# Kernel optimization log

Measured on AMD Instinct MI355X. Metric: run time of the kernel, lower is better.

## Reference

```python
import jax, jax.numpy as jnp
import numpy as np

B, S, D = 2, 2048, 2048
H = 16
Q_LORA, KV_LORA = 1536, 512
D_NOPE, D_ROPE, D_V = 128, 64, 128
QK_D = D_NOPE + D_ROPE  # 192
EPS = 1e-6
ROPE_THETA = 10000.0


def rms_norm(x, w, eps=EPS):
    return x * jax.lax.rsqrt(jnp.mean(x * x, axis=-1, keepdims=True) + eps) * w


def apply_rope(x, cos, sin):
    # x: [b, s, h, d]; cos/sin: [s, d//2]; pairs are interleaved (x0,x1),(x2,x3),...
    xr, xi = x[..., 0::2], x[..., 1::2]
    c = cos[None, :, None, :]
    s = sin[None, :, None, :]
    yr = xr * c - xi * s
    yi = xr * s + xi * c
    return jnp.stack([yr, yi], axis=-1).reshape(x.shape)


def setup_inputs() -> dict:
    key = jax.random.key(0)
    ks = jax.random.split(key, 8)
    sd = 0.02
    pos = jnp.arange(S, dtype=jnp.float32)
    inv_freq = 1.0 / (ROPE_THETA ** (jnp.arange(0, D_ROPE, 2, dtype=jnp.float32) / D_ROPE))
    ang = pos[:, None] * inv_freq[None, :]  # [S, D_ROPE//2]
    mask = jnp.triu(jnp.full((S, S), float('-inf'), dtype=jnp.float32), k=1)
    return {
        'x': jax.random.normal(ks[0], (B, S, D), dtype=jnp.float32),
        'freqs_cos': jnp.cos(ang),
        'freqs_sin': jnp.sin(ang),
        'mask': mask,
        'wq_a': jax.random.normal(ks[1], (Q_LORA, D), dtype=jnp.float32) * sd,
        'q_norm_w': jnp.ones((Q_LORA,), dtype=jnp.float32),
        'wq_b': jax.random.normal(ks[2], (H * QK_D, Q_LORA), dtype=jnp.float32) * sd,
        'wkv_a': jax.random.normal(ks[3], (KV_LORA + D_ROPE, D), dtype=jnp.float32) * sd,
        'kv_norm_w': jnp.ones((KV_LORA,), dtype=jnp.float32),
        'wkv_b': jax.random.normal(ks[4], (H * (D_NOPE + D_V), KV_LORA), dtype=jnp.float32) * sd,
        'wo': jax.random.normal(ks[5], (D, H * D_V), dtype=jnp.float32) * sd,
    }


def reference(x, freqs_cos, freqs_sin, mask, wq_a, q_norm_w, wq_b, wkv_a, kv_norm_w, wkv_b, wo):
    b, s, _ = x.shape
    # query path: down-proj -> RMSNorm -> up-proj
    q = rms_norm(x @ wq_a.T, q_norm_w) @ wq_b.T          # [b, s, H*QK_D]
    q = q.reshape(b, s, H, QK_D)
    q_nope, q_pe = q[..., :D_NOPE], q[..., D_NOPE:]
    q_pe = apply_rope(q_pe, freqs_cos, freqs_sin)
    # kv path: joint down-proj, split latent / rope key
    kv_full = x @ wkv_a.T                                 # [b, s, KV_LORA + D_ROPE]
    kv, k_pe = kv_full[..., :KV_LORA], kv_full[..., KV_LORA:]
    k_pe = apply_rope(k_pe[:, :, None, :], freqs_cos, freqs_sin)  # [b, s, 1, D_ROPE]
    q = jnp.concatenate([q_nope, q_pe], axis=-1)          # [b, s, H, QK_D]
    kv = rms_norm(kv, kv_norm_w) @ wkv_b.T                # [b, s, H*(D_NOPE+D_V)]
    kv = kv.reshape(b, s, H, D_NOPE + D_V)
    k_nope, v = kv[..., :D_NOPE], kv[..., D_NOPE:]
    k = jnp.concatenate([k_nope, jnp.broadcast_to(k_pe, (b, s, H, D_ROPE))], axis=-1)
    scale = QK_D ** -0.5
    scores = jnp.einsum('bshd,bthd->bsht', q, k) * scale + mask[None, :, None, :]
    probs = jax.nn.softmax(scores.astype(jnp.float32), axis=-1).astype(x.dtype)
    out = jnp.einsum('bsht,bthd->bshd', probs, v).reshape(b, s, H * D_V)
    return out @ wo.T
```

## Files before the change

### kernel.cpp

```cpp
#include <hip/hip_runtime.h>
#include <hip/hip_bf16.h>

typedef __bf16 bf16_t;
typedef __bf16 bf16x8 __attribute__((ext_vector_type(8)));
typedef __bf16 bf16x4 __attribute__((ext_vector_type(4)));
typedef __bf16 bf16x2 __attribute__((ext_vector_type(2)));
typedef float  f32x4  __attribute__((ext_vector_type(4)));
typedef float  f32x16 __attribute__((ext_vector_type(16)));

#define NB 2
#define NS 2048
#define ND 2048
#define NH 16
#define QLORA 1536
#define KVLORA 512
#define DNOPE 128
#define DROPE 64
#define DVDIM 128
#define QKD 192

#define QSCALE 0.10411754f

#if __has_builtin(__builtin_amdgcn_exp2f)
#define EXP2F(x) __builtin_amdgcn_exp2f(x)
#else
#define EXP2F(x) __expf((x) * 0.69314718056f)
#endif
#if __has_builtin(__builtin_amdgcn_rcpf)
#define RCPF(x) __builtin_amdgcn_rcpf(x)
#else
#define RCPF(x) (1.0f / (x))
#endif

typedef __attribute__((address_space(3))) void as3_void;
typedef __attribute__((address_space(1))) const void as1_void;
__device__ __forceinline__ void gload16(const void* g, void* l) {
  __builtin_amdgcn_global_load_lds((as1_void*)g, (as3_void*)l, 16, 0, 0);
}

__device__ __forceinline__ int pack2(float a, float b) {
  bf16x2 t = {(bf16_t)a, (bf16_t)b};
  return __builtin_bit_cast(int, t);
}

__global__ __launch_bounds__(256) void k_cvt_all(
    const float* __restrict__ x, const float* __restrict__ wqa,
    const float* __restrict__ wqb, const float* __restrict__ wkva,
    const float* __restrict__ wkvb, const float* __restrict__ wo,
    bf16_t* __restrict__ xb, bf16_t* __restrict__ wqab, bf16_t* __restrict__ wqbb,
    bf16_t* __restrict__ wkvab, bf16_t* __restrict__ wkvbb, bf16_t* __restrict__ wob) {
  const int c0 = 2097152, c1 = 2883584, c2 = 4063232, c3 = 4358144, c4 = 4882432,
            c5 = 5931008;
  int i = blockIdx.x * 256 + threadIdx.x;
  for (; i < c5; i += gridDim.x * 256) {
    const float* src;
    bf16_t* dst;
    int off;
    if (i < c0) { src = x; dst = xb; off = i; }
    else if (i < c1) { src = wqa; dst = wqab; off = i - c0; }
    else if (i < c2) { src = wqb; dst = wqbb; off = i - c1; }
    else if (i < c3) { src = wkva; dst = wkvab; off = i - c2; }
    else if (i < c4) { src = wkvb; dst = wkvbb; off = i - c3; }
    else { src = wo; dst = wob; off = i - c4; }
    float4 v = reinterpret_cast<const float4*>(src)[off];
    bf16x4 o = {(bf16_t)v.x, (bf16_t)v.y, (bf16_t)v.z, (bf16_t)v.w};
    reinterpret_cast<bf16x4*>(dst)[off] = o;
  }
}

template <int EPI>
__global__ __launch_bounds__(256) void k_gemm_bt(
    const bf16_t* __restrict__ A, const bf16_t* __restrict__ Bw,
    float* __restrict__ Cf, float* __restrict__ Cf2,
    bf16_t* __restrict__ Kout, bf16_t* __restrict__ Vtout,
    const float* __restrict__ fc, const float* __restrict__ fs,
    int M, int N, int K) {
  __shared__ bf16_t As[2][128 * 64];
  __shared__ bf16_t Bs[2][128 * 64];
  const int tid = threadIdx.x;
  const int lane = tid & 63;
  const int wave = tid >> 6;
  const int wm = (wave >> 1) * 64, wn = (wave & 1) * 64;
  const int m0 = blockIdx.y * 128, n0 = blockIdx.x * 128;
  const int l15 = lane & 15, l4 = lane >> 4;
  const int srow = lane >> 3;
  const int scol = ((lane & 7) ^ srow) * 8;

  const f32x4 Z4 = {0.f, 0.f, 0.f, 0.f};
  f32x4 acc[4][4];
#pragma unroll
  for (int i = 0; i < 4; ++i)
#pragma unroll
    for (int j = 0; j < 4; ++j) acc[i][j] = Z4;

  auto stage = [&](int buf, int k0) {
#pragma unroll
    for (int c = 0; c < 4; ++c) {
      int chunk = c * 4 + wave;
      int row = chunk * 8 + srow;
      gload16(A + (size_t)(m0 + row) * K + k0 + scol, &As[buf][chunk * 512]);
      gload16(Bw + (size_t)(n0 + row) * K + k0 + scol, &Bs[buf][chunk * 512]);
    }
  };

  const int nk = K >> 6;
  stage(0, 0);
  int cur = 0;
#pragma unroll 1
  for (int t = 0; t < nk; ++t) {
    if (t + 1 < nk) {
      stage(cur ^ 1, (t + 1) * 64);
      asm volatile("s_waitcnt vmcnt(8)" ::: "memory");
    } else {
      asm volatile("s_waitcnt vmcnt(0)" ::: "memory");
    }
    __builtin_amdgcn_sched_barrier(0);
    __builtin_amdgcn_s_barrier();
    __builtin_amdgcn_sched_barrier(0);
#pragma unroll
    for (int ks = 0; ks < 2; ++ks) {
      int kc = ks * 4 + l4;
      int pc = (kc ^ (l15 & 7)) * 8;
      bf16x8 af[4], bfr[4];
#pragma unroll
      for (int f = 0; f < 4; ++f) {
        af[f] = *reinterpret_cast<const bf16x8*>(&As[cur][(wm + f * 16 + l15) * 64 + pc]);
        bfr[f] = *reinterpret_cast<const bf16x8*>(&Bs[cur][(wn + f * 16 + l15) * 64 + pc]);
      }
#pragma unroll
      for (int fi = 0; fi < 4; ++fi)
#pragma unroll
        for (int fj = 0; fj < 4; ++fj)
          acc[fi][fj] = __builtin_amdgcn_mfma_f32_16x16x32_bf16(af[fi], bfr[fj], acc[fi][fj], 0, 0, 0);
    }
    __builtin_amdgcn_sched_barrier(0);
    __builtin_amdgcn_s_barrier();
    cur ^= 1;
  }

#pragma unroll
  for (int fi = 0; fi < 4; ++fi) {
#pragma unroll
    for (int fj = 0; fj < 4; ++fj) {
      int col = n0 + wn + fj * 16 + l15;
#pragma unroll
      for (int r = 0; r < 4; ++r) {
        int row = m0 + wm + fi * 16 + l4 * 4 + r;
        float v = acc[fi][fj][r];
        if (EPI == 0) {
          if (col < N) Cf[(size_t)row * N + col] = v;
        } else if (EPI == 1) {
          int h = col >> 8, rr = col & 255;
          int b = row >> 11, s = row & 2047;
          if (rr < DNOPE)
            Kout[(((size_t)(b * NH + h)) * NS + s) * QKD + rr] = (bf16_t)v;
          else
            Vtout[(((size_t)(b * NH + h)) * DVDIM + (rr - DNOPE)) * NS + s] = (bf16_t)v;
        } else if (EPI == 2) {
          int h = col / 192;
          int d = col - h * 192;
          int b = row >> 11, s = row & 2047;
          float y = v;
          if (d >= DNOPE) {
            float pv = __shfl_xor(v, 1);
            int pp = ((d & ~1) - DNOPE) >> 1;
            float c = fc[s * 32 + pp], si = fs[s * 32 + pp];
            y = (col & 1) ? (pv * si + v * c) : (v * c - pv * si);
          }
          Kout[((size_t)(b * NH + h) * NS + s) * QKD + d] = (bf16_t)(y * QSCALE);
        } else {
          if (col < QLORA) Cf[(size_t)row * QLORA + col] = v;
          else if (col < QLORA + KVLORA + DROPE)
            Cf2[(size_t)row * (KVLORA + DROPE) + (col - QLORA)] = v;
        }
      }
    }
  }
}

template <int COLS>
__global__ __launch_bounds__(256) void k_rmsnorm(const float* __restrict__ in,
                                                 const float* __restrict__ w,
                                                 bf16_t* __restrict__ out) {
  int row = blockIdx.x;
  const float* rp = in + (size_t)row * COLS;
  float ss = 0.f;
  for (int c = threadIdx.x * 4; c < COLS; c += 1024) {
    float4 v = *reinterpret_cast<const float4*>(rp + c);
    ss += v.x * v.x + v.y * v.y + v.z * v.z + v.w * v.w;
  }
#pragma unroll
  for (int m = 32; m; m >>= 1) ss += __shfl_xor(ss, m);
  __shared__ float red[4];
  if ((threadIdx.x & 63) == 0) red[threadIdx.x >> 6] = ss;
  __syncthreads();
  float tot = red[0] + red[1] + red[2] + red[3];
  float rs = rsqrtf(tot / (float)COLS + 1e-6f);
  for (int c = threadIdx.x * 4; c < COLS; c += 1024) {
    float4 v = *reinterpret_cast<const float4*>(rp + c);
    bf16x4 o = {(bf16_t)(v.x * rs * w[c]), (bf16_t)(v.y * rs * w[c + 1]),
                (bf16_t)(v.z * rs * w[c + 2]), (bf16_t)(v.w * rs * w[c + 3])};
    *reinterpret_cast<bf16x4*>(out + (size_t)row * COLS + c) = o;
  }
}

__global__ __launch_bounds__(256) void k_kv_post(const float* __restrict__ kvf,
                                                 const float* __restrict__ w,
                                                 const float* __restrict__ fc,
                                                 const float* __restrict__ fs,
                                                 bf16_t* __restrict__ kvn,
                                                 bf16_t* __restrict__ Kb) {
  int row = blockIdx.x;
  const float* rp = kvf + (size_t)row * (KVLORA + DROPE);
  float ss = 0.f;
  float4 v = {0.f, 0.f, 0.f, 0.f};
  if (threadIdx.x < 128) {
    v = reinterpret_cast<const float4*>(rp)[threadIdx.x];
    ss = v.x * v.x + v.y * v.y + v.z * v.z + v.w * v.w;
  }
#pragma unroll
  for (int m = 32; m; m >>= 1) ss += __shfl_xor(ss, m);
  __shared__ float red[4];
  if ((threadIdx.x & 63) == 0) red[threadIdx.x >> 6] = ss;
  __syncthreads();
  float tot = red[0] + red[1] + red[2] + red[3];
  float rs = rsqrtf(tot / (float)KVLORA + 1e-6f);
  if (threadIdx.x < 128) {
    int c = threadIdx.x * 4;
    bf16x4 o = {(bf16_t)(v.x * rs * w[c]), (bf16_t)(v.y * rs * w[c + 1]),
                (bf16_t)(v.z * rs * w[c + 2]), (bf16_t)(v.w * rs * w[c + 3])};
    *reinterpret_cast<bf16x4*>(kvn + (size_t)row * KVLORA + c) = o;
  }
  int b = row >> 11, s = row & 2047;
  if (threadIdx.x < 32) {
    int p = threadIdx.x;
    float x0 = rp[KVLORA + 2 * p], x1 = rp[KVLORA + 2 * p + 1];
    float c = fc[s * 32 + p], si = fs[s * 32 + p];
    float yr = x0 * c - x1 * si, yi = x0 * si + x1 * c;
    bf16_t br = (bf16_t)yr, bi = (bf16_t)yi;
    for (int h = 0; h < NH; ++h) {
      size_t ob = ((size_t)(b * NH + h) * NS + s) * QKD + DNOPE;
      Kb[ob + 2 * p] = br;
      Kb[ob + 2 * p + 1] = bi;
    }
  }
}

__global__ __launch_bounds__(256, 2) void k_attn(const bf16_t* __restrict__ Qb,
                                                 const bf16_t* __restrict__ Kb,
                                                 const bf16_t* __restrict__ Vtb,
                                                 bf16_t* __restrict__ Ao) {
  __shared__ bf16x8 Ks8[2][64 * 24];
  __shared__ bf16x8 Vs8[2][128 * 8];
  const int id = blockIdx.x;
  const int bh = id & 31;
  const int aa = (id >> 5) & 7;
  const int qt = (id >> 8) ? aa : (15 - aa);
  const int b = bh >> 4, h = bh & 15;
  const int tid = threadIdx.x;
  const int lane = tid & 63, wave = tid >> 6;
  const int l31 = lane & 31, hi = lane >> 5;
  const int q0w = qt * 128 + wave * 32;
  const int qg = q0w + l31;
  const int c4 = hi * 4;
  const int ntiles = 2 * qt + 2;
  const size_t bhNS = (size_t)bh * NS;

  const bf16_t* KbB = Kb + bhNS * QKD;
  const bf16_t* VtB = Vtb + (size_t)bh * DVDIM * NS;
  int koff[6], voff[4];
#pragma unroll
  for (int i = 0; i < 6; ++i) {
    int p = tid + i * 256;
    int row = p / 24, pc = p % 24;
    int lc = (pc & ~7) | ((pc ^ row) & 7);
    koff[i] = row * QKD + lc * 8;
  }
#pragma unroll
  for (int i = 0; i < 4; ++i) {
    int p = tid + i * 256;
    int row = p >> 3, pc = p & 7;
    int lc = pc ^ (row & 7);
    voff[i] = row * NS + lc * 8;
  }

  auto stageKV = [&](int buf, int kv0) {
    const bf16_t* ksrc = KbB + kv0 * QKD;
    const bf16_t* vsrc = VtB + kv0;
    bf16x8* kdst = &Ks8[buf][wave * 64];
    bf16x8* vdst = &Vs8[buf][wave * 64];
#pragma unroll
    for (int i = 0; i < 6; ++i) gload16(ksrc + koff[i], kdst + i * 256);
#pragma unroll
    for (int i = 0; i < 4; ++i) gload16(vsrc + voff[i], vdst + i * 256);
  };

  bf16x8 qf[12];
  {
    const bf16_t* qp = Qb + (bhNS + qg) * QKD + hi * 8;
#pragma unroll
    for (int ks = 0; ks < 12; ++ks)
      qf[ks] = *reinterpret_cast<const bf16x8*>(qp + ks * 16);
  }

  f32x16 oacc[4];
#pragma unroll
  for (int d = 0; d < 4; ++d) oacc[d] = {};
  float mrun = -3e38f, lrun = 0.f;

  stageKV(0, 0);
  int cur = 0;

#pragma unroll 1
  for (int kt = 0; kt < ntiles; ++kt) {
    const int kv0 = kt * 64;
    if (kt + 1 < ntiles) {
      stageKV(cur ^ 1, kv0 + 64);
      asm volatile("s_waitcnt vmcnt(10)" ::: "memory");
    } else {
      asm volatile("s_waitcnt vmcnt(0)" ::: "memory");
    }
    __builtin_amdgcn_sched_barrier(0);
    __builtin_amdgcn_s_barrier();
    __builtin_amdgcn_sched_barrier(0);

    if (kv0 <= q0w + 31) {
      f32x16 sacc[2];
      sacc[0] = {};
      sacc[1] = {};
#pragma unroll
      for (int ks = 0; ks < 12; ++ks) {
#pragma unroll
        for (int kh = 0; kh < 2; ++kh) {
          int row = kh * 32 + l31;
          int c = ks * 2 + hi;
          int pc = (c & ~7) | ((c ^ row) & 7);
          sacc[kh] = __builtin_amdgcn_mfma_f32_32x32x16_bf16(Ks8[cur][row * 24 + pc],
                                                             qf[ks], sacc[kh], 0, 0, 0);
        }
      }

      const bool diag = (kv0 + 63 > q0w);
      float mloc = -3e38f;
#pragma unroll
      for (int kh = 0; kh < 2; ++kh)
#pragma unroll
        for (int rg = 0; rg < 16; ++rg) {
          float s = sacc[kh][rg];
          if (diag) {
            int kg = kv0 + kh * 32 + (rg & 3) + 8 * (rg >> 2) + c4;
            if (kg > qg) s = -3e38f;
            sacc[kh][rg] = s;
          }
          mloc = fmaxf(mloc, s);
        }
      mloc = fmaxf(mloc, __shfl_xor(mloc, 32));

      if (!__all(mloc <= mrun)) {
        float mn = fmaxf(mrun, mloc);
        float fac = EXP2F(mrun - mn);
        mrun = mn;
        lrun *= fac;
#pragma unroll
        for (int d = 0; d < 4; ++d)
#pragma unroll
          for (int rg = 0; rg < 16; ++rg) oacc[d][rg] *= fac;
      }

      float rsum = 0.f;
      int W[8][2];
#pragma unroll
      for (int kh = 0; kh < 2; ++kh)
#pragma unroll
        for (int g = 0; g < 4; ++g) {
          float p0 = EXP2F(sacc[kh][4 * g + 0] - mrun);
          float p1 = EXP2F(sacc[kh][4 * g + 1] - mrun);
          float p2 = EXP2F(sacc[kh][4 * g + 2] - mrun);
          float p3 = EXP2F(sacc[kh][4 * g + 3] - mrun);
          rsum += (p0 + p1) + (p2 + p3);
          W[kh * 4 + g][0] = pack2(p0, p1);
          W[kh * 4 + g][1] = pack2(p2, p3);
        }
      rsum += __shfl_xor(rsum, 32);
      lrun += rsum;

      bf16x8 pa[4];
#pragma unroll
      for (int pks = 0; pks < 4; ++pks) {
        int kh = pks >> 1, G0 = (pks & 1) * 2;
        int a0 = W[kh * 4 + G0][0], a1 = W[kh * 4 + G0][1];
        int b0 = W[kh * 4 + G0 + 1][0], b1 = W[kh * 4 + G0 + 1][1];
        int own0 = hi ? b0 : a0, own1 = hi ? b1 : a1;
        int oth0 = hi ? a0 : b0, oth1 = hi ? a1 : b1;
        int rc0 = __shfl_xor(oth0, 32), rc1 = __shfl_xor(oth1, 32);
        int4 wv;
        wv.x = hi ? rc0 : own0;
        wv.y = hi ? rc1 : own1;
        wv.z = hi ? own0 : rc0;
        wv.w = hi ? own1 : rc1;
        pa[pks] = __builtin_bit_cast(bf16x8, wv);
      }

#pragma unroll
      for (int pks = 0; pks < 4; ++pks)
#pragma unroll
        for (int dvt = 0; dvt < 4; ++dvt) {
          int row = dvt * 32 + l31;
          int pc = (pks * 2 + hi) ^ (row & 7);
          oacc[dvt] = __builtin_amdgcn_mfma_f32_32x32x16_bf16(Vs8[cur][row * 8 + pc],
                                                              pa[pks], oacc[dvt], 0, 0, 0);
        }
    }

    __builtin_amdgcn_sched_barrier(0);
    __builtin_amdgcn_s_barrier();
    cur ^= 1;
  }

  float lr = RCPF(lrun);
  bf16_t* base = Ao + ((size_t)(b * NS) + qg) * (NH * DVDIM) + h * DVDIM;
#pragma unroll
  for (int dvt = 0; dvt < 4; ++dvt)
#pragma unroll
    for (int rg4 = 0; rg4 < 4; ++rg4) {
      int dv0 = dvt * 32 + 8 * rg4 + c4;
      bf16x4 o = {(bf16_t)(oacc[dvt][rg4 * 4 + 0] * lr),
                  (bf16_t)(oacc[dvt][rg4 * 4 + 1] * lr),
                  (bf16_t)(oacc[dvt][rg4 * 4 + 2] * lr),
                  (bf16_t)(oacc[dvt][rg4 * 4 + 3] * lr)};
      *reinterpret_cast<bf16x4*>(base + dv0) = o;
    }
}

extern "C" void kernel_launch(void* const* d_in, const int* in_sizes, int n_in,
                              void* d_out, int out_size, void* d_ws, size_t ws_size,
                              hipStream_t stream) {
  (void)in_sizes; (void)n_in; (void)out_size; (void)ws_size;
  const float* x = (const float*)d_in[0];
  const float* fcos = (const float*)d_in[1];
  const float* fsin = (const float*)d_in[2];
  const float* wq_a = (const float*)d_in[4];
  const float* q_norm_w = (const float*)d_in[5];
  const float* wq_b = (const float*)d_in[6];
  const float* wkv_a = (const float*)d_in[7];
  const float* kv_norm_w = (const float*)d_in[8];
  const float* wkv_b = (const float*)d_in[9];
  const float* wo = (const float*)d_in[10];
  float* out = (float*)d_out;

  char* p = (char*)d_ws;
  bf16_t* x_bf = (bf16_t*)(p);
  bf16_t* wqa_bf = (bf16_t*)(p + 16777216);
  bf16_t* wkva_bf = (bf16_t*)(p + 23068672);
  bf16_t* wqb_bf = (bf16_t*)(p + 25427968);
  bf16_t* wkvb_bf = (bf16_t*)(p + 34865152);
  bf16_t* wo_bf = (bf16_t*)(p + 39059456);
  float* qa_f32 = (float*)(p + 47448064);
  bf16_t* Kb = (bf16_t*)(p + 47448064);
  bf16_t* qan_bf = (bf16_t*)(p + 72613888);
  bf16_t* Qb = (bf16_t*)(p + 85196800);
  char* r2 = p + 110362624;
  float* kvf_f32 = (float*)(r2);
  bf16_t* kvn_bf = (bf16_t*)(r2 + 9437184);
  bf16_t* Vtb = (bf16_t*)(r2 + 13631488);
  bf16_t* attn_bf = (bf16_t*)(r2 + 30408704);

  k_cvt_all<<<2048, 256, 0, stream>>>(x, wq_a, wq_b, wkv_a, wkv_b, wo, x_bf, wqa_bf,
                                      wqb_bf, wkva_bf, wkvb_bf, wo_bf);

  k_gemm_bt<3><<<dim3(17, 32), 256, 0, stream>>>(x_bf, wqa_bf, qa_f32, kvf_f32,
                                                 nullptr, nullptr, nullptr, nullptr,
                                                 NB * NS, QLORA + KVLORA + DROPE, ND);
  k_rmsnorm<QLORA><<<NB * NS, 256, 0, stream>>>(qa_f32, q_norm_w, qan_bf);
  k_kv_post<<<NB * NS, 256, 0, stream>>>(kvf_f32, kv_norm_w, fcos, fsin, kvn_bf, Kb);
  k_gemm_bt<2><<<dim3(24, 32), 256, 0, stream>>>(qan_bf, wqb_bf, nullptr, nullptr, Qb,
                                                 nullptr, fcos, fsin, NB * NS, NH * QKD,
                                                 QLORA);
  k_gemm_bt<1><<<dim3(32, 32), 256, 0, stream>>>(kvn_bf, wkvb_bf, nullptr, nullptr, Kb,
                                                 Vtb, nullptr, nullptr, NB * NS,
                                                 NH * (DNOPE + DVDIM), KVLORA);
  k_attn<<<dim3(512), 256, 0, stream>>>(Qb, Kb, Vtb, attn_bf);
  k_gemm_bt<0><<<dim3(16, 32), 256, 0, stream>>>(attn_bf, wo_bf, out, nullptr, nullptr,
                                                 nullptr, nullptr, nullptr, NB * NS, ND,
                                                 NH * DVDIM);
}
```

Before: 363.8 us.

## Remap GEMM blocks across XCDs, vectorize V-transpose stores, fuse norms, add MFMA priority

GEMM launches become 1D grids whose block ids are remapped so that consecutive tiles land on the same XCD, aiming at better L2 reuse of the shared operand tiles. The EPI==1 epilogue writes transposed V as packed bf16x4 instead of scattered scalar stores. The q RMSNorm and kv post-processing kernels are merged into one launch to save a kernel launch and its scheduling gap. s_setprio is placed around the attention MFMA loops to favour matrix issue across waves. The remap assumes gridDim.x is divisible by 8, which holds for 544, 768, 1024 and 512.

```diff
diff --git a/kernel.cpp b/kernel.cpp
--- a/kernel.cpp
+++ b/kernel.cpp
@@ -81,7 +81,11 @@
   const int lane = tid & 63;
   const int wave = tid >> 6;
   const int wm = (wave >> 1) * 64, wn = (wave & 1) * 64;
-  const int m0 = blockIdx.y * 128, n0 = blockIdx.x * 128;
+  const int nxt = (N + 127) >> 7;
+  const int per = gridDim.x >> 3;
+  const int rank = (blockIdx.x & 7) * per + (blockIdx.x >> 3);
+  const int by = rank / nxt, bx = rank - by * nxt;
+  const int m0 = by * 128, n0 = bx * 128;
   const int l15 = lane & 15, l4 = lane >> 4;
   const int srow = lane >> 3;
   const int scol = ((lane & 7) ^ srow) * 8;
@@ -143,74 +147,82 @@
 #pragma unroll
     for (int fj = 0; fj < 4; ++fj) {
       int col = n0 + wn + fj * 16 + l15;
-#pragma unroll
-      for (int r = 0; r < 4; ++r) {
-        int row = m0 + wm + fi * 16 + l4 * 4 + r;
-        float v = acc[fi][fj][r];
-        if (EPI == 0) {
-          if (col < N) Cf[(size_t)row * N + col] = v;
-        } else if (EPI == 1) {
-          int h = col >> 8, rr = col & 255;
-          int b = row >> 11, s = row & 2047;
-          if (rr < DNOPE)
-            Kout[(((size_t)(b * NH + h)) * NS + s) * QKD + rr] = (bf16_t)v;
-          else
-            Vtout[(((size_t)(b * NH + h)) * DVDIM + (rr - DNOPE)) * NS + s] = (bf16_t)v;
-        } else if (EPI == 2) {
-          int h = col / 192;
-          int d = col - h * 192;
-          int b = row >> 11, s = row & 2047;
-          float y = v;
-          if (d >= DNOPE) {
-            float pv = __shfl_xor(v, 1);
-            int pp = ((d & ~1) - DNOPE) >> 1;
-            float c = fc[s * 32 + pp], si = fs[s * 32 + pp];
-            y = (col & 1) ? (pv * si + v * c) : (v * c - pv * si);
+      int row0 = m0 + wm + fi * 16 + l4 * 4;
+      if (EPI == 1) {
+        int h = col >> 8, rr = col & 255;
+        int b = row0 >> 11, s0 = row0 & 2047;
+        if (rr < DNOPE) {
+#pragma unroll
+          for (int r = 0; r < 4; ++r)
+            Kout[(((size_t)(b * NH + h)) * NS + s0 + r) * QKD + rr] =
+                (bf16_t)acc[fi][fj][r];
+        } else {
+          bf16x4 pv4 = {(bf16_t)acc[fi][fj][0], (bf16_t)acc[fi][fj][1],
+                        (bf16_t)acc[fi][fj][2], (bf16_t)acc[fi][fj][3]};
+          *reinterpret_cast<bf16x4*>(
+              &Vtout[(((size_t)(b * NH + h)) * DVDIM + (rr - DNOPE)) * NS + s0]) = pv4;
+        }
+      } else {
+#pragma unroll
+        for (int r = 0; r < 4; ++r) {
+          int row = row0 + r;
+          float v = acc[fi][fj][r];
+          if (EPI == 0) {
+            Cf[(size_t)row * N + col] = v;
+          } else if (EPI == 2) {
+            int h = col / 192;
+            int d = col - h * 192;
+            int b = row >> 11, s = row & 2047;
+            float y = v;
+            if (d >= DNOPE) {
+              float pv = __shfl_xor(v, 1);
+              int pp = ((d & ~1) - DNOPE) >> 1;
+              float c = fc[s * 32 + pp], si = fs[s * 32 + pp];
+              y = (col & 1) ? (pv * si + v * c) : (v * c - pv * si);
+            }
+            Kout[((size_t)(b * NH + h) * NS + s) * QKD + d] = (bf16_t)(y * QSCALE);
+          } else {
+            int b = row >> 11;
+            (void)b;
+            if (col < QLORA) Cf[(size_t)row * QLORA + col] = v;
+            else if (col < QLORA + KVLORA + DROPE)
+              Cf2[(size_t)row * (KVLORA + DROPE) + (col - QLORA)] = v;
           }
-          Kout[((size_t)(b * NH + h) * NS + s) * QKD + d] = (bf16_t)(y * QSCALE);
-        } else {
-          if (col < QLORA) Cf[(size_t)row * QLORA + col] = v;
-          else if (col < QLORA + KVLORA + DROPE)
-            Cf2[(size_t)row * (KVLORA + DROPE) + (col - QLORA)] = v;
         }
       }
     }
   }
 }
 
-template <int COLS>
-__global__ __launch_bounds__(256) void k_rmsnorm(const float* __restrict__ in,
-                                                 const float* __restrict__ w,
-                                                 bf16_t* __restrict__ out) {
+__global__ __launch_bounds__(256) void k_norm_post(
+    const float* __restrict__ qa, const float* __restrict__ qw,
+    bf16_t* __restrict__ qan, const float* __restrict__ kvf,
+    const float* __restrict__ kw, const float* __restrict__ fc,
+    const float* __restrict__ fs, bf16_t* __restrict__ kvn,
+    bf16_t* __restrict__ Kb) {
   int row = blockIdx.x;
-  const float* rp = in + (size_t)row * COLS;
-  float ss = 0.f;
-  for (int c = threadIdx.x * 4; c < COLS; c += 1024) {
-    float4 v = *reinterpret_cast<const float4*>(rp + c);
-    ss += v.x * v.x + v.y * v.y + v.z * v.z + v.w * v.w;
-  }
-#pragma unroll
-  for (int m = 32; m; m >>= 1) ss += __shfl_xor(ss, m);
   __shared__ float red[4];
-  if ((threadIdx.x & 63) == 0) red[threadIdx.x >> 6] = ss;
+  {
+    const float* rp = qa + (size_t)row * QLORA;
+    float ss = 0.f;
+    for (int c = threadIdx.x * 4; c < QLORA; c += 1024) {
+      float4 v = *reinterpret_cast<const float4*>(rp + c);
+      ss += v.x * v.x + v.y * v.y + v.z * v.z + v.w * v.w;
+    }
+#pragma unroll
+    for (int m = 32; m; m >>= 1) ss += __shfl_xor(ss, m);
+    if ((threadIdx.x & 63) == 0) red[threadIdx.x >> 6] = ss;
+    __syncthreads();
+    float tot = red[0] + red[1] + red[2] + red[3];
+    float rs = rsqrtf(tot / (float)QLORA + 1e-6f);
+    for (int c = threadIdx.x * 4; c < QLORA; c += 1024) {
+      float4 v = *reinterpret_cast<const float4*>(rp + c);
+      bf16x4 o = {(bf16_t)(v.x * rs * qw[c]), (bf16_t)(v.y * rs * qw[c + 1]),
+                  (bf16_t)(v.z * rs * qw[c + 2]), (bf16_t)(v.w * rs * qw[c + 3])};
+      *reinterpret_cast<bf16x4*>(qan + (size_t)row * QLORA + c) = o;
+    }
+  }
   __syncthreads();
-  float tot = red[0] + red[1] + red[2] + red[3];
-  float rs = rsqrtf(tot / (float)COLS + 1e-6f);
-  for (int c = threadIdx.x * 4; c < COLS; c += 1024) {
-    float4 v = *reinterpret_cast<const float4*>(rp + c);
-    bf16x4 o = {(bf16_t)(v.x * rs * w[c]), (bf16_t)(v.y * rs * w[c + 1]),
-                (bf16_t)(v.z * rs * w[c + 2]), (bf16_t)(v.w * rs * w[c + 3])};
-    *reinterpret_cast<bf16x4*>(out + (size_t)row * COLS + c) = o;
-  }
-}
-
-__global__ __launch_bounds__(256) void k_kv_post(const float* __restrict__ kvf,
-                                                 const float* __restrict__ w,
-                                                 const float* __restrict__ fc,
-                                                 const float* __restrict__ fs,
-                                                 bf16_t* __restrict__ kvn,
-                                                 bf16_t* __restrict__ Kb) {
-  int row = blockIdx.x;
   const float* rp = kvf + (size_t)row * (KVLORA + DROPE);
   float ss = 0.f;
   float4 v = {0.f, 0.f, 0.f, 0.f};
@@ -220,15 +232,14 @@
   }
 #pragma unroll
   for (int m = 32; m; m >>= 1) ss += __shfl_xor(ss, m);
-  __shared__ float red[4];
   if ((threadIdx.x & 63) == 0) red[threadIdx.x >> 6] = ss;
   __syncthreads();
   float tot = red[0] + red[1] + red[2] + red[3];
   float rs = rsqrtf(tot / (float)KVLORA + 1e-6f);
   if (threadIdx.x < 128) {
     int c = threadIdx.x * 4;
-    bf16x4 o = {(bf16_t)(v.x * rs * w[c]), (bf16_t)(v.y * rs * w[c + 1]),
-                (bf16_t)(v.z * rs * w[c + 2]), (bf16_t)(v.w * rs * w[c + 3])};
+    bf16x4 o = {(bf16_t)(v.x * rs * kw[c]), (bf16_t)(v.y * rs * kw[c + 1]),
+                (bf16_t)(v.z * rs * kw[c + 2]), (bf16_t)(v.w * rs * kw[c + 3])};
     *reinterpret_cast<bf16x4*>(kvn + (size_t)row * KVLORA + c) = o;
   }
   int b = row >> 11, s = row & 2047;
@@ -328,6 +339,7 @@
       f32x16 sacc[2];
       sacc[0] = {};
       sacc[1] = {};
+      __builtin_amdgcn_s_setprio(1);
 #pragma unroll
       for (int ks = 0; ks < 12; ++ks) {
 #pragma unroll
@@ -339,6 +351,7 @@
                                                              qf[ks], sacc[kh], 0, 0, 0);
         }
       }
+      __builtin_amdgcn_s_setprio(0);
 
       const bool diag = (kv0 + 63 > q0w);
       float mloc = -3e38f;
@@ -401,6 +414,7 @@
         pa[pks] = __builtin_bit_cast(bf16x8, wv);
       }
 
+      __builtin_amdgcn_s_setprio(1);
 #pragma unroll
       for (int pks = 0; pks < 4; ++pks)
 #pragma unroll
@@ -410,6 +424,7 @@
           oacc[dvt] = __builtin_amdgcn_mfma_f32_32x32x16_bf16(Vs8[cur][row * 8 + pc],
                                                               pa[pks], oacc[dvt], 0, 0, 0);
         }
+      __builtin_amdgcn_s_setprio(0);
     }
 
     __builtin_amdgcn_sched_barrier(0);
@@ -468,19 +483,19 @@
   k_cvt_all<<<2048, 256, 0, stream>>>(x, wq_a, wq_b, wkv_a, wkv_b, wo, x_bf, wqa_bf,
                                       wqb_bf, wkva_bf, wkvb_bf, wo_bf);
 
-  k_gemm_bt<3><<<dim3(17, 32), 256, 0, stream>>>(x_bf, wqa_bf, qa_f32, kvf_f32,
-                                                 nullptr, nullptr, nullptr, nullptr,
-                                                 NB * NS, QLORA + KVLORA + DROPE, ND);
-  k_rmsnorm<QLORA><<<NB * NS, 256, 0, stream>>>(qa_f32, q_norm_w, qan_bf);
-  k_kv_post<<<NB * NS, 256, 0, stream>>>(kvf_f32, kv_norm_w, fcos, fsin, kvn_bf, Kb);
-  k_gemm_bt<2><<<dim3(24, 32), 256, 0, stream>>>(qan_bf, wqb_bf, nullptr, nullptr, Qb,
-                                                 nullptr, fcos, fsin, NB * NS, NH * QKD,
-                                                 QLORA);
-  k_gemm_bt<1><<<dim3(32, 32), 256, 0, stream>>>(kvn_bf, wkvb_bf, nullptr, nullptr, Kb,
-                                                 Vtb, nullptr, nullptr, NB * NS,
-                                                 NH * (DNOPE + DVDIM), KVLORA);
+  k_gemm_bt<3><<<dim3(544), 256, 0, stream>>>(x_bf, wqa_bf, qa_f32, kvf_f32,
+                                              nullptr, nullptr, nullptr, nullptr,
+                                              NB * NS, QLORA + KVLORA + DROPE, ND);
+  k_norm_post<<<NB * NS, 256, 0, stream>>>(qa_f32, q_norm_w, qan_bf, kvf_f32,
+                                           kv_norm_w, fcos, fsin, kvn_bf, Kb);
+  k_gemm_bt<2><<<dim3(768), 256, 0, stream>>>(qan_bf, wqb_bf, nullptr, nullptr, Qb,
+                                              nullptr, fcos, fsin, NB * NS, NH * QKD,
+                                              QLORA);
+  k_gemm_bt<1><<<dim3(1024), 256, 0, stream>>>(kvn_bf, wkvb_bf, nullptr, nullptr, Kb,
+                                               Vtb, nullptr, nullptr, NB * NS,
+                                               NH * (DNOPE + DVDIM), KVLORA);
   k_attn<<<dim3(512), 256, 0, stream>>>(Qb, Kb, Vtb, attn_bf);
-  k_gemm_bt<0><<<dim3(16, 32), 256, 0, stream>>>(attn_bf, wo_bf, out, nullptr, nullptr,
-                                                 nullptr, nullptr, nullptr, NB * NS, ND,
-                                                 NH * DVDIM);
-}
+  k_gemm_bt<0><<<dim3(512), 256, 0, stream>>>(attn_bf, wo_bf, out, nullptr, nullptr,
+                                              nullptr, nullptr, nullptr, NB * NS, ND,
+                                              NH * DVDIM);
+}
```

After: 349.2 us. 1.04x faster.
